# Performance work log

Hardware: AMD Instinct MI355X
Metric: run time of the kernel (lower is better)

Reference implementation:

```python
import jax, jax.numpy as jnp
import numpy as np

N, Z, E, M0, M1, D = 16384, 100, 400, 4000, 2000, 4


def setup_inputs() -> dict:
    key = jax.random.key(0)
    k = jax.random.split(key, 7)
    return {
        "theta": jax.random.normal(k[0], (N, Z), jnp.float32),
        "alpha0": jax.random.normal(k[1], (M0, E), jnp.float32),
        "alpha1": jax.random.normal(k[2], (M1, E), jnp.float32),
        "beta": jax.random.normal(k[3], (Z, E), jnp.float32),
        "bias0": jax.random.normal(k[4], (D, M0), jnp.float32),
        "bias1": jax.random.normal(k[5], (D, M1), jnp.float32),
        "domain_idx": jax.random.randint(k[6], (N,), 0, D, dtype=jnp.int32),
    }


def _recon_mod(theta, alpha, beta, bias, domain_idx):
    # Topic_mod = (alpha @ beta.T).T == beta @ alpha.T : (Z, M)
    topic = beta @ alpha.T
    # per-domain GEMM + indexed bias-add + log_softmax + scatter-back
    # == single GEMM with per-row gathered bias (all domains present)
    logits = theta @ topic + bias[domain_idx]  # (N, M)
    return jax.nn.log_softmax(logits, axis=-1)


def reference(theta, alpha0, alpha1, beta, bias0, bias1, domain_idx):
    r0 = _recon_mod(theta, alpha0, beta, bias0, domain_idx)
    r1 = _recon_mod(theta, alpha1, beta, bias1, domain_idx)
    return (r0, r1)
```

## Files before the change

### kernel.cpp

```cpp
#include <hip/hip_runtime.h>
#include <hip/hip_bf16.h>

#define PN 16384
#define PZ 100
#define PE 400
#define PM0 4000
#define PM1 2000
#define KP 128
#define SEG1ROW 4096
#define MROWS 6144

typedef __attribute__((ext_vector_type(8))) _Float16 half8v;
typedef __attribute__((ext_vector_type(4))) float floatx4;
typedef __attribute__((ext_vector_type(4))) unsigned int uint4v;

__device__ __forceinline__ void gload16(const void* g, void* l) {
    __builtin_amdgcn_global_load_lds(
        (const __attribute__((address_space(1))) void*)g,
        (__attribute__((address_space(3))) void*)l, 16, 0, 0);
}

__global__ __launch_bounds__(256) void fill_kernel(uint4v* __restrict__ p, int n16)
{
    int i = blockIdx.x * 256 + threadIdx.x;
    if (i < n16) p[i] = (uint4v){0u, 0u, 0u, 0u};
}

__global__ __launch_bounds__(256) void topic_kernel(
    const float* __restrict__ alpha0, const float* __restrict__ alpha1,
    const float* __restrict__ beta, _Float16* __restrict__ b2t)
{
    const int seg = (blockIdx.x >= 64);
    const int tile = seg ? (blockIdx.x - 64) : blockIdx.x;
    const float* alpha = seg ? alpha1 : alpha0;
    const int M = seg ? PM1 : PM0;
    const int rowbase = seg ? SEG1ROW : 0;

    __shared__ float sA[64][201];
    const int tid = threadIdx.x;
    const int ml = tid & 63;
    const int zt = tid >> 6;
    const int m0 = tile * 64;
    const int z0 = blockIdx.y * 20 + zt * 5;

    float acc[5] = {0.f, 0.f, 0.f, 0.f, 0.f};

    for (int ec = 0; ec < 2; ++ec) {
        #pragma unroll
        for (int l = 0; l < 50; ++l) {
            int idx = tid + l * 256;
            int mr = idx / 200;
            int e  = idx - mr * 200;
            int m  = m0 + mr;
            sA[mr][e] = (m < M) ? alpha[(size_t)m * PE + ec * 200 + e] : 0.f;
        }
        __syncthreads();
        const float* bz = beta + (size_t)z0 * PE + ec * 200;
        #pragma unroll 4
        for (int e = 0; e < 200; ++e) {
            float a = sA[ml][e];
            #pragma unroll
            for (int zi = 0; zi < 5; ++zi)
                acc[zi] = fmaf(bz[zi * PE + e], a, acc[zi]);
        }
        __syncthreads();
    }
    int m = m0 + ml;
    if (m < M) {
        #pragma unroll
        for (int zi = 0; zi < 5; ++zi)
            b2t[(size_t)(rowbase + m) * KP + (z0 + zi)] = (_Float16)acc[zi];
    }
}

__global__ __launch_bounds__(256, 4) void fused_kernel(
    const float* __restrict__ theta,
    const _Float16* __restrict__ B2T,
    const float* __restrict__ bias0, const float* __restrict__ bias1,
    const int* __restrict__ dom,
    float* __restrict__ out0, float* __restrict__ out1)
{
    __shared__ __align__(1024) char sAreg[8192];
    __shared__ __align__(1024) _Float16 sB[2][64 * 128];

    int*   sdom = (int*)sAreg;
    float* swx  = (float*)(sAreg + 128);
    float* sws  = (float*)(sAreg + 128 + 512);
    float* slse = (float*)(sAreg + 128 + 1024);

    const int tid = threadIdx.x;
    const int w   = tid >> 6;
    const int ll  = tid & 63;
    const int g   = ll >> 4;
    const int c   = ll & 15;

    const int seg = blockIdx.x & 1;
    const int n0  = (blockIdx.x >> 1) * 32;
    const int M   = seg ? PM1 : PM0;
    const int NT  = seg ? 32 : 63;
    const _Float16* Bseg = B2T + (size_t)(seg ? SEG1ROW : 0) * KP;
    const float* bias = seg ? bias1 : bias0;
    float* out = seg ? out1 : out0;

    #pragma unroll
    for (int p = 0; p < 2; ++p) {
        int idx  = tid + p * 256;
        int row  = idx >> 4;
        int slot = idx & 15;
        const float* tr = theta + (size_t)(n0 + row) * PZ + slot * 8;
        half8v h;
        if (slot < 12) {
            float4 lo = *(const float4*)tr;
            float4 hi = *(const float4*)(tr + 4);
            h[0] = (_Float16)lo.x; h[1] = (_Float16)lo.y;
            h[2] = (_Float16)lo.z; h[3] = (_Float16)lo.w;
            h[4] = (_Float16)hi.x; h[5] = (_Float16)hi.y;
            h[6] = (_Float16)hi.z; h[7] = (_Float16)hi.w;
        } else if (slot == 12) {
            float4 lo = *(const float4*)tr;
            h[0] = (_Float16)lo.x; h[1] = (_Float16)lo.y;
            h[2] = (_Float16)lo.z; h[3] = (_Float16)lo.w;
            h[4] = (_Float16)0.f; h[5] = (_Float16)0.f;
            h[6] = (_Float16)0.f; h[7] = (_Float16)0.f;
        } else {
            h = (half8v)(_Float16)0.f;
        }
        *(half8v*)(sAreg + row * 256 + ((slot ^ (row & 7)) * 16)) = h;
    }

    const int srow  = ll >> 4;
    const int sslot = ll & 15;
    auto stageB = [&](int buf, int t) {
        #pragma unroll
        for (int it = 0; it < 4; ++it) {
            int row  = w * 16 + it * 4 + srow;
            int slot = sslot ^ (row & 7);
            gload16(Bseg + ((size_t)t * 64 + row) * KP + slot * 8,
                    (char*)&sB[buf][0] + (w * 16 + it * 4) * 256);
        }
    };

    stageB(0, 0);
    __syncthreads();

    half8v aF[2][4];
    #pragma unroll
    for (int mi = 0; mi < 2; ++mi) {
        int row = mi * 16 + c;
        #pragma unroll
        for (int kb = 0; kb < 4; ++kb) {
            int slot = (kb * 4 + g) ^ (row & 7);
            aF[mi][kb] = *(const half8v*)(sAreg + row * 256 + slot * 16);
        }
    }
    __syncthreads();
    if (tid < 32) sdom[tid] = dom[n0 + tid];
    __syncthreads();

    float mx_[2][4], sm_[2][4];
    #pragma unroll
    for (int mi = 0; mi < 2; ++mi)
        #pragma unroll
        for (int i = 0; i < 4; ++i) { mx_[mi][i] = -3.0e38f; sm_[mi][i] = 0.f; }

    for (int t = 0; t < NT; ++t) {
        if (t) __syncthreads();
        if (t + 1 < NT) stageB((t + 1) & 1, t + 1);

        half8v bF[4];
        const int brow = w * 16 + c;
        #pragma unroll
        for (int kb = 0; kb < 4; ++kb) {
            int slot = (kb * 4 + g) ^ (brow & 7);
            bF[kb] = *(const half8v*)((const char*)&sB[t & 1][0] + brow * 256 + slot * 16);
        }

        floatx4 acc[2];
        acc[0] = (floatx4){0.f, 0.f, 0.f, 0.f};
        acc[1] = (floatx4){0.f, 0.f, 0.f, 0.f};
        #pragma unroll
        for (int mi = 0; mi < 2; ++mi)
            #pragma unroll
            for (int kb = 0; kb < 4; ++kb)
                acc[mi] = __builtin_amdgcn_mfma_f32_16x16x32_f16(
                    aF[mi][kb], bF[kb], acc[mi], 0, 0, 0);

        const int m  = t * 64 + w * 16 + c;
        const bool mv = (m < M);
        const int mc = mv ? m : (M - 1);
        float bv0 = bias[0 * (size_t)M + mc];
        float bv1 = bias[1 * (size_t)M + mc];
        float bv2 = bias[2 * (size_t)M + mc];
        float bv3 = bias[3 * (size_t)M + mc];

        #pragma unroll
        for (int mi = 0; mi < 2; ++mi) {
            #pragma unroll
            for (int i = 0; i < 4; ++i) {
                int row = mi * 16 + 4 * g + i;
                int d = sdom[row];
                float bv = (d < 2) ? (d == 0 ? bv0 : bv1) : (d == 2 ? bv2 : bv3);
                float v = mv ? (acc[mi][i] + bv) : -3.0e38f;
                float nm = fmaxf(mx_[mi][i], v);
                sm_[mi][i] = sm_[mi][i] * __expf(mx_[mi][i] - nm) + __expf(v - nm);
                mx_[mi][i] = nm;
            }
        }
    }

    #pragma unroll
    for (int mi = 0; mi < 2; ++mi) {
        #pragma unroll
        for (int i = 0; i < 4; ++i) {
            float m_ = mx_[mi][i], s_ = sm_[mi][i];
            #pragma unroll
            for (int msk = 1; msk < 16; msk <<= 1) {
                float mo = __shfl_xor(m_, msk);
                float so = __shfl_xor(s_, msk);
                float nm = fmaxf(m_, mo);
                s_ = s_ * __expf(m_ - nm) + so * __expf(mo - nm);
                m_ = nm;
            }
            if (c == 0) {
                int row = mi * 16 + 4 * g + i;
                swx[w * 32 + row] = m_;
                sws[w * 32 + row] = s_;
            }
        }
    }
    __syncthreads();

    stageB(0, 0);

    if (tid < 32) {
        float m_ = swx[tid], s_ = sws[tid];
        #pragma unroll
        for (int wv = 1; wv < 4; ++wv) {
            float mo = swx[wv * 32 + tid];
            float so = sws[wv * 32 + tid];
            float nm = fmaxf(m_, mo);
            s_ = s_ * __expf(m_ - nm) + so * __expf(mo - nm);
            m_ = nm;
        }
        slse[tid] = m_ + __logf(s_);
    }
    __syncthreads();

    for (int t = 0; t < NT; ++t) {
        if (t) __syncthreads();
        if (t + 1 < NT) stageB((t + 1) & 1, t + 1);

        half8v bF[4];
        const int brow = w * 16 + c;
        #pragma unroll
        for (int kb = 0; kb < 4; ++kb) {
            int slot = (kb * 4 + g) ^ (brow & 7);
            bF[kb] = *(const half8v*)((const char*)&sB[t & 1][0] + brow * 256 + slot * 16);
        }

        floatx4 acc[2];
        acc[0] = (floatx4){0.f, 0.f, 0.f, 0.f};
        acc[1] = (floatx4){0.f, 0.f, 0.f, 0.f};
        #pragma unroll
        for (int mi = 0; mi < 2; ++mi)
            #pragma unroll
            for (int kb = 0; kb < 4; ++kb)
                acc[mi] = __builtin_amdgcn_mfma_f32_16x16x32_f16(
                    aF[mi][kb], bF[kb], acc[mi], 0, 0, 0);

        const int m  = t * 64 + w * 16 + c;
        const bool mv = (m < M);
        const int mc = mv ? m : (M - 1);
        float bv0 = bias[0 * (size_t)M + mc];
        float bv1 = bias[1 * (size_t)M + mc];
        float bv2 = bias[2 * (size_t)M + mc];
        float bv3 = bias[3 * (size_t)M + mc];

        if (mv) {
            #pragma unroll
            for (int mi = 0; mi < 2; ++mi) {
                #pragma unroll
                for (int i = 0; i < 4; ++i) {
                    int row = mi * 16 + 4 * g + i;
                    int d = sdom[row];
                    float bv = (d < 2) ? (d == 0 ? bv0 : bv1) : (d == 2 ? bv2 : bv3);
                    float o = acc[mi][i] + bv - slse[row];
                    __builtin_nontemporal_store(o, &out[(size_t)(n0 + row) * M + m]);
                }
            }
        }
    }
}

extern "C" void kernel_launch(void* const* d_in, const int* in_sizes, int n_in,
                              void* d_out, int out_size, void* d_ws, size_t ws_size,
                              hipStream_t stream) {
    const float* theta  = (const float*)d_in[0];
    const float* alpha0 = (const float*)d_in[1];
    const float* alpha1 = (const float*)d_in[2];
    const float* beta   = (const float*)d_in[3];
    const float* bias0  = (const float*)d_in[4];
    const float* bias1  = (const float*)d_in[5];
    const int*   dom    = (const int*)d_in[6];

    float* out0 = (float*)d_out;
    float* out1 = out0 + (size_t)PN * PM0;

    _Float16* B2T = (_Float16*)d_ws;

    {
        int n16 = MROWS * KP * 2 / 16;
        fill_kernel<<<(n16 + 255) / 256, 256, 0, stream>>>((uint4v*)B2T, n16);
    }

    topic_kernel<<<dim3(96, 5), 256, 0, stream>>>(alpha0, alpha1, beta, B2T);

    fused_kernel<<<(PN / 32) * 2, 256, 0, stream>>>(
        theta, B2T, bias0, bias1, dom, out0, out1);
}
```

Before: 303.7 us.

## Drop LDS staging of B, widen blocks to 512 threads, skip softmax rescale

The fused kernel no longer stages B tiles into LDS with async global-to-LDS loads and barriers. Each wave now reads its B fragments straight from global memory (L2-resident) and skips per-tile syncs. One 512-thread block now handles both output segments for its 32 rows instead of a separate block per segment. The online softmax skips the max-rescale exp when new values stay within a threshold of the running max, and domain ids live in registers. This trades barrier and LDS traffic for direct global loads that may have more latency and less coalescing.

```diff
diff --git a/kernel.cpp b/kernel.cpp
--- a/kernel.cpp
+++ b/kernel.cpp
@@ -13,12 +13,6 @@
 typedef __attribute__((ext_vector_type(8))) _Float16 half8v;
 typedef __attribute__((ext_vector_type(4))) float floatx4;
 typedef __attribute__((ext_vector_type(4))) unsigned int uint4v;
-
-__device__ __forceinline__ void gload16(const void* g, void* l) {
-    __builtin_amdgcn_global_load_lds(
-        (const __attribute__((address_space(1))) void*)g,
-        (__attribute__((address_space(3))) void*)l, 16, 0, 0);
-}
 
 __global__ __launch_bounds__(256) void fill_kernel(uint4v* __restrict__ p, int n16)
 {
@@ -73,40 +67,28 @@
     }
 }
 
-__global__ __launch_bounds__(256, 4) void fused_kernel(
+__global__ __launch_bounds__(512, 4) void fused_kernel(
     const float* __restrict__ theta,
     const _Float16* __restrict__ B2T,
     const float* __restrict__ bias0, const float* __restrict__ bias1,
     const int* __restrict__ dom,
     float* __restrict__ out0, float* __restrict__ out1)
 {
-    __shared__ __align__(1024) char sAreg[8192];
-    __shared__ __align__(1024) _Float16 sB[2][64 * 128];
-
-    int*   sdom = (int*)sAreg;
-    float* swx  = (float*)(sAreg + 128);
-    float* sws  = (float*)(sAreg + 128 + 512);
-    float* slse = (float*)(sAreg + 128 + 1024);
+    __shared__ __align__(1024) char sA[8192];
+    __shared__ float smx[8][32];
+    __shared__ float sms[8][32];
+    __shared__ float slse[32];
 
     const int tid = threadIdx.x;
     const int w   = tid >> 6;
     const int ll  = tid & 63;
     const int g   = ll >> 4;
     const int c   = ll & 15;
-
-    const int seg = blockIdx.x & 1;
-    const int n0  = (blockIdx.x >> 1) * 32;
-    const int M   = seg ? PM1 : PM0;
-    const int NT  = seg ? 32 : 63;
-    const _Float16* Bseg = B2T + (size_t)(seg ? SEG1ROW : 0) * KP;
-    const float* bias = seg ? bias1 : bias0;
-    float* out = seg ? out1 : out0;
-
-    #pragma unroll
-    for (int p = 0; p < 2; ++p) {
-        int idx  = tid + p * 256;
-        int row  = idx >> 4;
-        int slot = idx & 15;
+    const int n0  = blockIdx.x * 32;
+
+    {
+        int row  = tid >> 4;
+        int slot = tid & 15;
         const float* tr = theta + (size_t)(n0 + row) * PZ + slot * 8;
         half8v h;
         if (slot < 12) {
@@ -125,22 +107,8 @@
         } else {
             h = (half8v)(_Float16)0.f;
         }
-        *(half8v*)(sAreg + row * 256 + ((slot ^ (row & 7)) * 16)) = h;
-    }
-
-    const int srow  = ll >> 4;
-    const int sslot = ll & 15;
-    auto stageB = [&](int buf, int t) {
-        #pragma unroll
-        for (int it = 0; it < 4; ++it) {
-            int row  = w * 16 + it * 4 + srow;
-            int slot = sslot ^ (row & 7);
-            gload16(Bseg + ((size_t)t * 64 + row) * KP + slot * 8,
-                    (char*)&sB[buf][0] + (w * 16 + it * 4) * 256);
-        }
-    };
-
-    stageB(0, 0);
+        *(half8v*)(sA + row * 256 + ((slot ^ (row & 7)) * 16)) = h;
+    }
     __syncthreads();
 
     half8v aF[2][4];
@@ -150,142 +118,172 @@
         #pragma unroll
         for (int kb = 0; kb < 4; ++kb) {
             int slot = (kb * 4 + g) ^ (row & 7);
-            aF[mi][kb] = *(const half8v*)(sAreg + row * 256 + slot * 16);
-        }
-    }
-    __syncthreads();
-    if (tid < 32) sdom[tid] = dom[n0 + tid];
-    __syncthreads();
-
-    float mx_[2][4], sm_[2][4];
+            aF[mi][kb] = *(const half8v*)(sA + row * 256 + slot * 16);
+        }
+    }
+
+    int drow[2][4];
     #pragma unroll
     for (int mi = 0; mi < 2; ++mi)
         #pragma unroll
-        for (int i = 0; i < 4; ++i) { mx_[mi][i] = -3.0e38f; sm_[mi][i] = 0.f; }
-
-    for (int t = 0; t < NT; ++t) {
-        if (t) __syncthreads();
-        if (t + 1 < NT) stageB((t + 1) & 1, t + 1);
-
-        half8v bF[4];
-        const int brow = w * 16 + c;
-        #pragma unroll
-        for (int kb = 0; kb < 4; ++kb) {
-            int slot = (kb * 4 + g) ^ (brow & 7);
-            bF[kb] = *(const half8v*)((const char*)&sB[t & 1][0] + brow * 256 + slot * 16);
-        }
-
-        floatx4 acc[2];
-        acc[0] = (floatx4){0.f, 0.f, 0.f, 0.f};
-        acc[1] = (floatx4){0.f, 0.f, 0.f, 0.f};
+        for (int i = 0; i < 4; ++i)
+            drow[mi][i] = dom[n0 + mi * 16 + 4 * g + i];
+
+    for (int seg = 0; seg < 2; ++seg) {
+        const int Mse = seg ? PM1 : PM0;
+        const int NT  = seg ? 16 : 32;
+        const _Float16* Bseg = B2T + (size_t)(seg ? SEG1ROW : 0) * KP;
+        const float* bias = seg ? bias1 : bias0;
+        float* out = seg ? out1 : out0;
+
+        const _Float16* bcol = Bseg + (size_t)(w * 16 + c) * KP;
+        const int mbase = w * 16 + c;
+
+        float mx_[2][4], sm_[2][4];
         #pragma unroll
         for (int mi = 0; mi < 2; ++mi)
             #pragma unroll
+            for (int i = 0; i < 4; ++i) { mx_[mi][i] = -3.0e38f; sm_[mi][i] = 0.f; }
+
+        for (int t = 0; t < NT; ++t) {
+            const int m  = t * 128 + mbase;
+            const _Float16* bp = bcol + (size_t)t * 128 * KP;
+            half8v bF[4];
+            #pragma unroll
             for (int kb = 0; kb < 4; ++kb)
-                acc[mi] = __builtin_amdgcn_mfma_f32_16x16x32_f16(
-                    aF[mi][kb], bF[kb], acc[mi], 0, 0, 0);
-
-        const int m  = t * 64 + w * 16 + c;
-        const bool mv = (m < M);
-        const int mc = mv ? m : (M - 1);
-        float bv0 = bias[0 * (size_t)M + mc];
-        float bv1 = bias[1 * (size_t)M + mc];
-        float bv2 = bias[2 * (size_t)M + mc];
-        float bv3 = bias[3 * (size_t)M + mc];
+                bF[kb] = *(const half8v*)(bp + kb * 32 + g * 8);
+
+            const bool mv = (m < Mse);
+            const int mc = mv ? m : (Mse - 1);
+            float bv0 = bias[mc];
+            float bv1 = bias[(size_t)Mse + mc];
+            float bv2 = bias[2 * (size_t)Mse + mc];
+            float bv3 = bias[3 * (size_t)Mse + mc];
+
+            floatx4 acc[2];
+            acc[0] = (floatx4){0.f, 0.f, 0.f, 0.f};
+            acc[1] = (floatx4){0.f, 0.f, 0.f, 0.f};
+            #pragma unroll
+            for (int mi = 0; mi < 2; ++mi)
+                #pragma unroll
+                for (int kb = 0; kb < 4; ++kb)
+                    acc[mi] = __builtin_amdgcn_mfma_f32_16x16x32_f16(
+                        aF[mi][kb], bF[kb], acc[mi], 0, 0, 0);
+
+            float vv[2][4];
+            float gm = -3.0e38f;
+            #pragma unroll
+            for (int mi = 0; mi < 2; ++mi) {
+                #pragma unroll
+                for (int i = 0; i < 4; ++i) {
+                    int d = drow[mi][i];
+                    float bv = (d < 2) ? (d == 0 ? bv0 : bv1) : (d == 2 ? bv2 : bv3);
+                    float v = mv ? (acc[mi][i] + bv) : -1.0e30f;
+                    vv[mi][i] = v;
+                    gm = fmaxf(gm, v - mx_[mi][i]);
+                }
+            }
+            if (gm <= 8.0f) {
+                #pragma unroll
+                for (int mi = 0; mi < 2; ++mi)
+                    #pragma unroll
+                    for (int i = 0; i < 4; ++i)
+                        sm_[mi][i] += __expf(vv[mi][i] - mx_[mi][i]);
+            } else {
+                #pragma unroll
+                for (int mi = 0; mi < 2; ++mi) {
+                    #pragma unroll
+                    for (int i = 0; i < 4; ++i) {
+                        float v  = vv[mi][i];
+                        float nm = fmaxf(mx_[mi][i], v);
+                        sm_[mi][i] = sm_[mi][i] * __expf(mx_[mi][i] - nm)
+                                   + __expf(v - nm);
+                        mx_[mi][i] = nm;
+                    }
+                }
+            }
+        }
 
         #pragma unroll
         for (int mi = 0; mi < 2; ++mi) {
             #pragma unroll
             for (int i = 0; i < 4; ++i) {
-                int row = mi * 16 + 4 * g + i;
-                int d = sdom[row];
-                float bv = (d < 2) ? (d == 0 ? bv0 : bv1) : (d == 2 ? bv2 : bv3);
-                float v = mv ? (acc[mi][i] + bv) : -3.0e38f;
-                float nm = fmaxf(mx_[mi][i], v);
-                sm_[mi][i] = sm_[mi][i] * __expf(mx_[mi][i] - nm) + __expf(v - nm);
-                mx_[mi][i] = nm;
-            }
-        }
-    }
-
-    #pragma unroll
-    for (int mi = 0; mi < 2; ++mi) {
-        #pragma unroll
-        for (int i = 0; i < 4; ++i) {
-            float m_ = mx_[mi][i], s_ = sm_[mi][i];
-            #pragma unroll
-            for (int msk = 1; msk < 16; msk <<= 1) {
-                float mo = __shfl_xor(m_, msk);
-                float so = __shfl_xor(s_, msk);
+                float m_ = mx_[mi][i], s_ = sm_[mi][i];
+                #pragma unroll
+                for (int msk = 1; msk < 16; msk <<= 1) {
+                    float mo = __shfl_xor(m_, msk);
+                    float so = __shfl_xor(s_, msk);
+                    float nm = fmaxf(m_, mo);
+                    s_ = s_ * __expf(m_ - nm) + so * __expf(mo - nm);
+                    m_ = nm;
+                }
+                if (c == 0) {
+                    int row = mi * 16 + 4 * g + i;
+                    smx[w][row] = m_;
+                    sms[w][row] = s_;
+                }
+            }
+        }
+        __syncthreads();
+        if (tid < 32) {
+            float m_ = smx[0][tid], s_ = sms[0][tid];
+            #pragma unroll
+            for (int wv = 1; wv < 8; ++wv) {
+                float mo = smx[wv][tid];
+                float so = sms[wv][tid];
                 float nm = fmaxf(m_, mo);
                 s_ = s_ * __expf(m_ - nm) + so * __expf(mo - nm);
                 m_ = nm;
             }
-            if (c == 0) {
-                int row = mi * 16 + 4 * g + i;
-                swx[w * 32 + row] = m_;
-                sws[w * 32 + row] = s_;
-            }
-        }
-    }
-    __syncthreads();
-
-    stageB(0, 0);
-
-    if (tid < 32) {
-        float m_ = swx[tid], s_ = sws[tid];
-        #pragma unroll
-        for (int wv = 1; wv < 4; ++wv) {
-            float mo = swx[wv * 32 + tid];
-            float so = sws[wv * 32 + tid];
-            float nm = fmaxf(m_, mo);
-            s_ = s_ * __expf(m_ - nm) + so * __expf(mo - nm);
-            m_ = nm;
-        }
-        slse[tid] = m_ + __logf(s_);
-    }
-    __syncthreads();
-
-    for (int t = 0; t < NT; ++t) {
-        if (t) __syncthreads();
-        if (t + 1 < NT) stageB((t + 1) & 1, t + 1);
-
-        half8v bF[4];
-        const int brow = w * 16 + c;
-        #pragma unroll
-        for (int kb = 0; kb < 4; ++kb) {
-            int slot = (kb * 4 + g) ^ (brow & 7);
-            bF[kb] = *(const half8v*)((const char*)&sB[t & 1][0] + brow * 256 + slot * 16);
-        }
-
-        floatx4 acc[2];
-        acc[0] = (floatx4){0.f, 0.f, 0.f, 0.f};
-        acc[1] = (floatx4){0.f, 0.f, 0.f, 0.f};
+            slse[tid] = m_ + __logf(s_);
+        }
+        __syncthreads();
+        float lse_[2][4];
         #pragma unroll
         for (int mi = 0; mi < 2; ++mi)
             #pragma unroll
+            for (int i = 0; i < 4; ++i)
+                lse_[mi][i] = slse[mi * 16 + 4 * g + i];
+        __syncthreads();
+
+        for (int t = 0; t < NT; ++t) {
+            const int m  = t * 128 + mbase;
+            const _Float16* bp = bcol + (size_t)t * 128 * KP;
+            half8v bF[4];
+            #pragma unroll
             for (int kb = 0; kb < 4; ++kb)
-                acc[mi] = __builtin_amdgcn_mfma_f32_16x16x32_f16(
-                    aF[mi][kb], bF[kb], acc[mi], 0, 0, 0);
-
-        const int m  = t * 64 + w * 16 + c;
-        const bool mv = (m < M);
-        const int mc = mv ? m : (M - 1);
-        float bv0 = bias[0 * (size_t)M + mc];
-        float bv1 = bias[1 * (size_t)M + mc];
-        float bv2 = bias[2 * (size_t)M + mc];
-        float bv3 = bias[3 * (size_t)M + mc];
-
-        if (mv) {
-            #pragma unroll
-            for (int mi = 0; mi < 2; ++mi) {
-                #pragma unroll
-                for (int i = 0; i < 4; ++i) {
-                    int row = mi * 16 + 4 * g + i;
-                    int d = sdom[row];
-                    float bv = (d < 2) ? (d == 0 ? bv0 : bv1) : (d == 2 ? bv2 : bv3);
-                    float o = acc[mi][i] + bv - slse[row];
-                    __builtin_nontemporal_store(o, &out[(size_t)(n0 + row) * M + m]);
+                bF[kb] = *(const half8v*)(bp + kb * 32 + g * 8);
+
+            const bool mv = (m < Mse);
+            const int mc = mv ? m : (Mse - 1);
+            float bv0 = bias[mc];
+            float bv1 = bias[(size_t)Mse + mc];
+            float bv2 = bias[2 * (size_t)Mse + mc];
+            float bv3 = bias[3 * (size_t)Mse + mc];
+
+            floatx4 acc[2];
+            acc[0] = (floatx4){0.f, 0.f, 0.f, 0.f};
+            acc[1] = (floatx4){0.f, 0.f, 0.f, 0.f};
+            #pragma unroll
+            for (int mi = 0; mi < 2; ++mi)
+                #pragma unroll
+                for (int kb = 0; kb < 4; ++kb)
+                    acc[mi] = __builtin_amdgcn_mfma_f32_16x16x32_f16(
+                        aF[mi][kb], bF[kb], acc[mi], 0, 0, 0);
+
+            if (mv) {
+                #pragma unroll
+                for (int mi = 0; mi < 2; ++mi) {
+                    #pragma unroll
+                    for (int i = 0; i < 4; ++i) {
+                        int row = mi * 16 + 4 * g + i;
+                        int d = drow[mi][i];
+                        float bv = (d < 2) ? (d == 0 ? bv0 : bv1)
+                                           : (d == 2 ? bv2 : bv3);
+                        float o = acc[mi][i] + bv - lse_[mi][i];
+                        __builtin_nontemporal_store(
+                            o, &out[(size_t)(n0 + row) * Mse + m]);
+                    }
                 }
             }
         }
@@ -315,6 +313,6 @@
 
     topic_kernel<<<dim3(96, 5), 256, 0, stream>>>(alpha0, alpha1, beta, B2T);
 
-    fused_kernel<<<(PN / 32) * 2, 256, 0, stream>>>(
+    fused_kernel<<<PN / 32, 512, 0, stream>>>(
         theta, B2T, bias0, bias1, dom, out0, out1);
 }
```

Measured after the change: 315.1 us. +3.8%, slower.
